# Kernel tuning notes

Measured on AMD Instinct MI355X. Metric: run time of the kernel, lower is better.

Reference implementation:

```python
import jax, jax.numpy as jnp
import numpy as np

TEMPERATURE = 0.5
EPS = 1e-12  # torch F.normalize eps


def setup_inputs() -> dict:
    key = jax.random.key(0)
    k1, k2 = jax.random.split(key)
    z_i = jax.random.normal(k1, (32, 128, 128), dtype=jnp.float32)
    z_j = jax.random.normal(k2, (32, 128, 128), dtype=jnp.float32)
    return {"z_i": z_i, "z_j": z_j}


def _l2_normalize(x):
    # matches torch F.normalize(dim=1): x / max(||x||, eps)
    n = jnp.sqrt(jnp.sum(x * x, axis=1, keepdims=True))
    return x / jnp.maximum(n, EPS)


def _off_diagonal(a):
    # rows of a with the diagonal removed, row-major order -> [n, n-1]
    n = a.shape[0]
    return a.reshape(-1)[:-1].reshape(n - 1, n + 1)[:, 1:].reshape(n, n - 1)


def reference(z_i, z_j):
    B, S, D = z_i.shape
    N = B * S
    zi = _l2_normalize(z_i.reshape(N, D))
    zj = _l2_normalize(z_j.reshape(N, D))
    r = jnp.concatenate([zi, zj], axis=0)              # [2N, D]
    sim = r @ r.T                                      # [2N, 2N]
    # positives: off-diagonals at +/-N (unaffected by the diag -inf fill)
    pos = jnp.concatenate([jnp.diagonal(sim, N), jnp.diagonal(sim, -N)])  # [2N]
    # negatives: all non-diagonal entries, row-major (== torch boolean-mask view)
    neg = _off_diagonal(sim)                           # [2N, 2N-1]
    logits = jnp.concatenate([pos[:, None], neg], axis=1) / TEMPERATURE  # [2N, 2N]
    # labels are all 0 -> CE(sum) / 2N == mean of -log_softmax[:, 0]
    loss = -jax.nn.log_softmax(logits, axis=1)[:, 0]
    return jnp.sum(loss) / (2 * N)
```

## Files before the change

### kernel.cpp

```cpp
#include <hip/hip_runtime.h>
#include <hip/hip_bf16.h>
#include <math.h>

#define NPAIR 4096
#define D 128
#define TWO_N 8192
#define NSLAB 32
#define ALPHA 1.6986436f

typedef float f32x4 __attribute__((ext_vector_type(4)));
typedef int i32x8 __attribute__((ext_vector_type(8)));

__device__ __forceinline__ void async_ld16(void* lds, const void* g) {
    __builtin_amdgcn_global_load_lds(
        (__attribute__((address_space(1))) const unsigned int*)g,
        (__attribute__((address_space(3))) unsigned int*)lds, 16, 0, 0);
}

__device__ __forceinline__ i32x8 mk8(uint4 lo, uint4 hi) {
    return (i32x8){(int)lo.x, (int)lo.y, (int)lo.z, (int)lo.w,
                   (int)hi.x, (int)hi.y, (int)hi.z, (int)hi.w};
}

__global__ __launch_bounds__(256) void norm_kernel(const float* __restrict__ zi,
                                                   const float* __restrict__ zj,
                                                   unsigned char* __restrict__ Rb,
                                                   float* __restrict__ pos,
                                                   float* __restrict__ out) {
    if (blockIdx.x == 0 && threadIdx.x == 0) out[0] = 0.f;
    int k = blockIdx.x * 4 + (threadIdx.x >> 6);
    int t = threadIdx.x & 63;
    const float2 a = *(const float2*)(zi + k * D + 2 * t);
    const float2 b = *(const float2*)(zj + k * D + 2 * t);
    float si = a.x * a.x + a.y * a.y;
    float sj = b.x * b.x + b.y * b.y;
    float dt = a.x * b.x + a.y * b.y;
    #pragma unroll
    for (int m = 1; m < 64; m <<= 1) {
        si += __shfl_xor(si, m, 64);
        sj += __shfl_xor(sj, m, 64);
        dt += __shfl_xor(dt, m, 64);
    }
    float ii = 1.0f / fmaxf(sqrtf(si), 1e-12f);
    float ij = 1.0f / fmaxf(sqrtf(sj), 1e-12f);
    if (t == 0) pos[k] = dt * ii * ij;
    ii *= ALPHA; ij *= ALPHA;
    int r0 = __builtin_amdgcn_cvt_pk_fp8_f32(a.x * ii, a.y * ii, 0, false);
    *(unsigned short*)(Rb + (size_t)k * 128 + 2 * t) = (unsigned short)r0;
    int r1 = __builtin_amdgcn_cvt_pk_fp8_f32(b.x * ij, b.y * ij, 0, false);
    *(unsigned short*)(Rb + (size_t)(k + NPAIR) * 128 + 2 * t) = (unsigned short)r1;
}

__global__ __launch_bounds__(256, 4) void simexp_kernel(const unsigned char* __restrict__ Rb,
                                                        float* __restrict__ rspart) {
    __shared__ uint4 Bs[4][3][128];
    const int bi = blockIdx.x >> 3;
    const int jc = blockIdx.x & 7;
    const int tid = threadIdx.x;
    const int wave = tid >> 6, lane = tid & 63;
    const int rp = lane & 15, q = lane >> 4;

    i32x8 afr[4];
    {
        const unsigned char* Ab = Rb + (size_t)(bi * 64 + rp) * 128 + q * 32;
        #pragma unroll
        for (int rt = 0; rt < 4; ++rt) {
            uint4 h0 = *(const uint4*)(Ab + rt * 16 * 128);
            uint4 h1 = *(const uint4*)(Ab + rt * 16 * 128 + 16);
            afr[rt] = mk8(h0, h1);
        }
    }

    const unsigned char* gslab = Rb + (size_t)(jc * 1024 + wave * 16) * 128;
    char* lpanel = (char*)&Bs[wave][0][0];
    const int laneoff = (lane >> 3) * 128 + (((lane & 7) ^ ((lane >> 3) & 7)) << 4);

    float rs[16];
    #pragma unroll
    for (int i = 0; i < 16; ++i) rs[i] = 0.f;

    #pragma unroll
    for (int j = 0; j < 2; ++j)
        #pragma unroll
        for (int d = 0; d < 2; ++d)
            async_ld16(lpanel + j * 2048 + d * 1024,
                       gslab + j * 8192 + d * 1024 + laneoff);

    const int diagbase = bi * 64 - jc * 1024;
    const int slot0 = rp * 8;
    const int sw = rp & 7;

    #pragma unroll
    for (int jt = 0; jt < 16; ++jt) {
        if (jt < 14) __builtin_amdgcn_s_waitcnt(0x0F72);
        else         __builtin_amdgcn_s_waitcnt(0x0F70);

        const int cur = jt % 3;
        const uint4* P = &Bs[wave][cur][0];
        uint4 u0 = P[slot0 + ((q * 2 + 0) ^ sw)];
        uint4 u1 = P[slot0 + ((q * 2 + 1) ^ sw)];
        i32x8 bfr = mk8(u0, u1);

        if (jt < 14) {
            const int nb = (jt + 2) % 3;
            #pragma unroll
            for (int d = 0; d < 2; ++d)
                async_ld16(lpanel + nb * 2048 + d * 1024,
                           gslab + (jt + 2) * 8192 + d * 1024 + laneoff);
        }

        f32x4 acc[4] = {};
        #pragma unroll
        for (int rt = 0; rt < 4; ++rt)
            acc[rt] = __builtin_amdgcn_mfma_scale_f32_16x16x128_f8f6f4(
                afr[rt], bfr, acc[rt],
                0, 0,
                0, 0x7F7F7F7F,
                0, 0x7F7F7F7F);

        if (jt * 64 == diagbase) {
            #pragma unroll
            for (int rt = 0; rt < 4; ++rt)
                #pragma unroll
                for (int r = 0; r < 4; ++r) {
                    int ro = rt * 16 + q * 4 + r;
                    int co = wave * 16 + rp;
                    float e = __builtin_amdgcn_exp2f(acc[rt][r]);
                    rs[rt * 4 + r] += (ro == co) ? 0.f : e;
                }
        } else {
            #pragma unroll
            for (int rt = 0; rt < 4; ++rt)
                #pragma unroll
                for (int r = 0; r < 4; ++r)
                    rs[rt * 4 + r] += __builtin_amdgcn_exp2f(acc[rt][r]);
        }
    }

    #pragma unroll
    for (int i = 0; i < 16; ++i) {
        float v = rs[i];
        v += __shfl_xor(v, 1, 64);
        v += __shfl_xor(v, 2, 64);
        v += __shfl_xor(v, 4, 64);
        v += __shfl_xor(v, 8, 64);
        rs[i] = v;
    }
    if (rp == 0) {
        const int slab = jc * 4 + wave;
        const int rowb = bi * 64 + q * 4;
        #pragma unroll
        for (int rt = 0; rt < 4; ++rt)
            #pragma unroll
            for (int r = 0; r < 4; ++r)
                rspart[slab * TWO_N + rowb + rt * 16 + r] = rs[rt * 4 + r];
    }
}

__global__ __launch_bounds__(256) void finalize_kernel(const float* __restrict__ rspart,
                                                       const float* __restrict__ pos,
                                                       float* __restrict__ out) {
    __shared__ float red[4];
    int tid = threadIdx.x;
    float local = 0.f;
    #pragma unroll
    for (int i = 0; i < 2; ++i) {
        int k = blockIdx.x * 512 + i * 256 + tid;
        float rsum = 0.f;
        #pragma unroll
        for (int p = 0; p < NSLAB; ++p) rsum += rspart[p * TWO_N + k];
        float ps = pos[k & (NPAIR - 1)];
        float p2 = ps + ps;
        local += logf(rsum + __expf(p2)) - p2;
    }
    #pragma unroll
    for (int m = 1; m < 64; m <<= 1) local += __shfl_xor(local, m, 64);
    if ((tid & 63) == 0) red[tid >> 6] = local;
    __syncthreads();
    if (tid == 0) {
        float s = red[0] + red[1] + red[2] + red[3];
        atomicAdd(out, s * (1.0f / (float)TWO_N));
    }
}

extern "C" void kernel_launch(void* const* d_in, const int* in_sizes, int n_in,
                              void* d_out, int out_size, void* d_ws, size_t ws_size,
                              hipStream_t stream) {
    const float* zi = (const float*)d_in[0];
    const float* zj = (const float*)d_in[1];
    char* ws = (char*)d_ws;
    unsigned char* Rb = (unsigned char*)ws;
    float* rspart = (float*)(ws + 1 * 1024 * 1024);
    float* pos = (float*)(ws + 2 * 1024 * 1024);

    norm_kernel<<<NPAIR / 4, 256, 0, stream>>>(zi, zj, Rb, pos, (float*)d_out);
    simexp_kernel<<<128 * 8, 256, 0, stream>>>(Rb, rspart);
    finalize_kernel<<<16, 256, 0, stream>>>(rspart, pos, (float*)d_out);
}
```

Measured before the change: 76.86 us.

## Deepen LDS prefetch, software-pipeline MFMA with exp epilog, vectorize norm and finalize

The similarity kernel gets a 4-deep LDS ring with a 3-tile prefetch distance. Its MFMA results are double-buffered so the exp/row-sum epilog of tile j-1 overlaps the MFMAs of tile j, with setprio raised around the MFMAs. The norm kernel uses float4 loads with 32-lane reductions and packs four fp8 values per store. The row-sum partials are transposed to row-major so finalize can read them with contiguous vector loads across 64 blocks. The extra LDS buffer and the doubled accumulators raise register and LDS pressure, which may reduce occupancy.

```diff
diff --git a/kernel.cpp b/kernel.cpp
--- a/kernel.cpp
+++ b/kernel.cpp
@@ -28,32 +28,34 @@
                                                    float* __restrict__ pos,
                                                    float* __restrict__ out) {
     if (blockIdx.x == 0 && threadIdx.x == 0) out[0] = 0.f;
-    int k = blockIdx.x * 4 + (threadIdx.x >> 6);
-    int t = threadIdx.x & 63;
-    const float2 a = *(const float2*)(zi + k * D + 2 * t);
-    const float2 b = *(const float2*)(zj + k * D + 2 * t);
-    float si = a.x * a.x + a.y * a.y;
-    float sj = b.x * b.x + b.y * b.y;
-    float dt = a.x * b.x + a.y * b.y;
-    #pragma unroll
-    for (int m = 1; m < 64; m <<= 1) {
-        si += __shfl_xor(si, m, 64);
-        sj += __shfl_xor(sj, m, 64);
-        dt += __shfl_xor(dt, m, 64);
+    int k = blockIdx.x * 8 + (threadIdx.x >> 5);
+    int t = threadIdx.x & 31;
+    const float4 a = *(const float4*)(zi + k * D + 4 * t);
+    const float4 b = *(const float4*)(zj + k * D + 4 * t);
+    float si = a.x * a.x + a.y * a.y + a.z * a.z + a.w * a.w;
+    float sj = b.x * b.x + b.y * b.y + b.z * b.z + b.w * b.w;
+    float dt = a.x * b.x + a.y * b.y + a.z * b.z + a.w * b.w;
+    #pragma unroll
+    for (int m = 1; m < 32; m <<= 1) {
+        si += __shfl_xor(si, m, 32);
+        sj += __shfl_xor(sj, m, 32);
+        dt += __shfl_xor(dt, m, 32);
     }
     float ii = 1.0f / fmaxf(sqrtf(si), 1e-12f);
     float ij = 1.0f / fmaxf(sqrtf(sj), 1e-12f);
     if (t == 0) pos[k] = dt * ii * ij;
     ii *= ALPHA; ij *= ALPHA;
     int r0 = __builtin_amdgcn_cvt_pk_fp8_f32(a.x * ii, a.y * ii, 0, false);
-    *(unsigned short*)(Rb + (size_t)k * 128 + 2 * t) = (unsigned short)r0;
+    r0 = __builtin_amdgcn_cvt_pk_fp8_f32(a.z * ii, a.w * ii, r0, true);
+    *(unsigned int*)(Rb + (size_t)k * 128 + 4 * t) = (unsigned int)r0;
     int r1 = __builtin_amdgcn_cvt_pk_fp8_f32(b.x * ij, b.y * ij, 0, false);
-    *(unsigned short*)(Rb + (size_t)(k + NPAIR) * 128 + 2 * t) = (unsigned short)r1;
+    r1 = __builtin_amdgcn_cvt_pk_fp8_f32(b.z * ij, b.w * ij, r1, true);
+    *(unsigned int*)(Rb + (size_t)(k + NPAIR) * 128 + 4 * t) = (unsigned int)r1;
 }
 
 __global__ __launch_bounds__(256, 4) void simexp_kernel(const unsigned char* __restrict__ Rb,
                                                         float* __restrict__ rspart) {
-    __shared__ uint4 Bs[4][3][128];
+    __shared__ uint4 Bs[4][4][128];
     const int bi = blockIdx.x >> 3;
     const int jc = blockIdx.x & 7;
     const int tid = threadIdx.x;
@@ -80,7 +82,7 @@
     for (int i = 0; i < 16; ++i) rs[i] = 0.f;
 
     #pragma unroll
-    for (int j = 0; j < 2; ++j)
+    for (int j = 0; j < 3; ++j)
         #pragma unroll
         for (int d = 0; d < 2; ++d)
             async_ld16(lpanel + j * 2048 + d * 1024,
@@ -90,42 +92,15 @@
     const int slot0 = rp * 8;
     const int sw = rp & 7;
 
-    #pragma unroll
-    for (int jt = 0; jt < 16; ++jt) {
-        if (jt < 14) __builtin_amdgcn_s_waitcnt(0x0F72);
-        else         __builtin_amdgcn_s_waitcnt(0x0F70);
-
-        const int cur = jt % 3;
-        const uint4* P = &Bs[wave][cur][0];
-        uint4 u0 = P[slot0 + ((q * 2 + 0) ^ sw)];
-        uint4 u1 = P[slot0 + ((q * 2 + 1) ^ sw)];
-        i32x8 bfr = mk8(u0, u1);
-
-        if (jt < 14) {
-            const int nb = (jt + 2) % 3;
-            #pragma unroll
-            for (int d = 0; d < 2; ++d)
-                async_ld16(lpanel + nb * 2048 + d * 1024,
-                           gslab + (jt + 2) * 8192 + d * 1024 + laneoff);
-        }
-
-        f32x4 acc[4] = {};
-        #pragma unroll
-        for (int rt = 0; rt < 4; ++rt)
-            acc[rt] = __builtin_amdgcn_mfma_scale_f32_16x16x128_f8f6f4(
-                afr[rt], bfr, acc[rt],
-                0, 0,
-                0, 0x7F7F7F7F,
-                0, 0x7F7F7F7F);
-
-        if (jt * 64 == diagbase) {
+    auto epilog = [&](int j, f32x4 (&a)[4]) {
+        if (j * 64 == diagbase) {
             #pragma unroll
             for (int rt = 0; rt < 4; ++rt)
                 #pragma unroll
                 for (int r = 0; r < 4; ++r) {
                     int ro = rt * 16 + q * 4 + r;
                     int co = wave * 16 + rp;
-                    float e = __builtin_amdgcn_exp2f(acc[rt][r]);
+                    float e = __builtin_amdgcn_exp2f(a[rt][r]);
                     rs[rt * 4 + r] += (ro == co) ? 0.f : e;
                 }
         } else {
@@ -133,9 +108,47 @@
             for (int rt = 0; rt < 4; ++rt)
                 #pragma unroll
                 for (int r = 0; r < 4; ++r)
-                    rs[rt * 4 + r] += __builtin_amdgcn_exp2f(acc[rt][r]);
-        }
-    }
+                    rs[rt * 4 + r] += __builtin_amdgcn_exp2f(a[rt][r]);
+        }
+    };
+
+    f32x4 acc[2][4];
+
+    #pragma unroll
+    for (int jt = 0; jt < 16; ++jt) {
+        if (jt <= 13)      __builtin_amdgcn_s_waitcnt(0x0F74);
+        else if (jt == 14) __builtin_amdgcn_s_waitcnt(0x0F72);
+        else               __builtin_amdgcn_s_waitcnt(0x0F70);
+
+        const uint4* P = &Bs[wave][jt & 3][0];
+        uint4 u0 = P[slot0 + ((q * 2 + 0) ^ sw)];
+        uint4 u1 = P[slot0 + ((q * 2 + 1) ^ sw)];
+        i32x8 bfr = mk8(u0, u1);
+
+        if (jt <= 12) {
+            const int nb = (jt + 3) & 3;
+            #pragma unroll
+            for (int d = 0; d < 2; ++d)
+                async_ld16(lpanel + nb * 2048 + d * 1024,
+                           gslab + (jt + 3) * 8192 + d * 1024 + laneoff);
+        }
+
+        f32x4* accC = acc[jt & 1];
+        __builtin_amdgcn_s_setprio(1);
+        #pragma unroll
+        for (int rt = 0; rt < 4; ++rt) {
+            f32x4 z = {0.f, 0.f, 0.f, 0.f};
+            accC[rt] = __builtin_amdgcn_mfma_scale_f32_16x16x128_f8f6f4(
+                afr[rt], bfr, z,
+                0, 0,
+                0, 0x7F7F7F7F,
+                0, 0x7F7F7F7F);
+        }
+        __builtin_amdgcn_s_setprio(0);
+
+        if (jt > 0) epilog(jt - 1, acc[(jt - 1) & 1]);
+    }
+    epilog(15, acc[1]);
 
     #pragma unroll
     for (int i = 0; i < 16; ++i) {
@@ -153,34 +166,29 @@
         for (int rt = 0; rt < 4; ++rt)
             #pragma unroll
             for (int r = 0; r < 4; ++r)
-                rspart[slab * TWO_N + rowb + rt * 16 + r] = rs[rt * 4 + r];
-    }
-}
-
-__global__ __launch_bounds__(256) void finalize_kernel(const float* __restrict__ rspart,
+                rspart[(size_t)(rowb + rt * 16 + r) * NSLAB + slab] = rs[rt * 4 + r];
+    }
+}
+
+__global__ __launch_bounds__(128) void finalize_kernel(const float* __restrict__ rspart,
                                                        const float* __restrict__ pos,
                                                        float* __restrict__ out) {
-    __shared__ float red[4];
+    __shared__ float red[2];
     int tid = threadIdx.x;
-    float local = 0.f;
-    #pragma unroll
-    for (int i = 0; i < 2; ++i) {
-        int k = blockIdx.x * 512 + i * 256 + tid;
-        float rsum = 0.f;
-        #pragma unroll
-        for (int p = 0; p < NSLAB; ++p) rsum += rspart[p * TWO_N + k];
-        float ps = pos[k & (NPAIR - 1)];
-        float p2 = ps + ps;
-        local += logf(rsum + __expf(p2)) - p2;
-    }
+    int k = blockIdx.x * 128 + tid;
+    const f32x4* v = (const f32x4*)(rspart + (size_t)k * NSLAB);
+    f32x4 s = v[0];
+    #pragma unroll
+    for (int p = 1; p < 8; ++p) s += v[p];
+    float rsum = s.x + s.y + s.z + s.w;
+    float ps = pos[k & (NPAIR - 1)];
+    float p2 = ps + ps;
+    float local = logf(rsum + __expf(p2)) - p2;
     #pragma unroll
     for (int m = 1; m < 64; m <<= 1) local += __shfl_xor(local, m, 64);
     if ((tid & 63) == 0) red[tid >> 6] = local;
     __syncthreads();
-    if (tid == 0) {
-        float s = red[0] + red[1] + red[2] + red[3];
-        atomicAdd(out, s * (1.0f / (float)TWO_N));
-    }
+    if (tid == 0) atomicAdd(out, (red[0] + red[1]) * (1.0f / (float)TWO_N));
 }
 
 extern "C" void kernel_launch(void* const* d_in, const int* in_sizes, int n_in,
@@ -193,7 +201,7 @@
     float* rspart = (float*)(ws + 1 * 1024 * 1024);
     float* pos = (float*)(ws + 2 * 1024 * 1024);
 
-    norm_kernel<<<NPAIR / 4, 256, 0, stream>>>(zi, zj, Rb, pos, (float*)d_out);
+    norm_kernel<<<NPAIR / 8, 256, 0, stream>>>(zi, zj, Rb, pos, (float*)d_out);
     simexp_kernel<<<128 * 8, 256, 0, stream>>>(Rb, rspart);
-    finalize_kernel<<<16, 256, 0, stream>>>(rspart, pos, (float*)d_out);
-}
+    finalize_kernel<<<64, 128, 0, stream>>>(rspart, pos, (float*)d_out);
+}
```

After: 117.2 us. 1.52x slower.
